# Optimization experiments

Hardware: AMD Instinct MI355X
Metric: run time of the kernel (lower is better)

Reference implementation:

```python
import jax, jax.numpy as jnp
import numpy as np

N = 131072          # total nodes per batched graph side
E = 524288          # total edges per batched graph side (avg degree 4)
B = 4096            # number of graph pairs
NPG = 32            # nodes per graph
NEG_SLOPE = 0.2
LN_EPS = 1e-5


def setup_inputs() -> dict:
    key = jax.random.key(0)
    ks = jax.random.split(key, 40)
    rn = lambda k, s, sc=0.05: jax.random.normal(k, s, dtype=jnp.float32) * sc
    inp = {}
    inp["feat1"] = jax.random.normal(ks[0], (N, 6), dtype=jnp.float32)
    inp["feat2"] = jax.random.normal(ks[1], (N, 6), dtype=jnp.float32)
    inp["llm_emb"] = jax.random.normal(ks[2], (B, 1024), dtype=jnp.float32)
    inp["src1"] = jax.random.randint(ks[3], (E,), 0, N, dtype=jnp.int32)
    inp["dst1"] = jax.random.randint(ks[4], (E,), 0, N, dtype=jnp.int32)
    inp["src2"] = jax.random.randint(ks[5], (E,), 0, N, dtype=jnp.int32)
    inp["dst2"] = jax.random.randint(ks[6], (E,), 0, N, dtype=jnp.int32)
    inp["gid"] = (jnp.arange(N, dtype=jnp.int32) // NPG).astype(jnp.int32)
    # shared GAT weights (layer: W[in,H*Dh], attn_l[H,Dh], attn_r[H,Dh], bias[H*Dh])
    inp["W1"] = rn(ks[7], (6, 128));   inp["al1"] = rn(ks[8], (4, 32));  inp["ar1"] = rn(ks[9], (4, 32));  inp["b1"] = rn(ks[10], (128,))
    inp["W2"] = rn(ks[11], (128, 128)); inp["al2"] = rn(ks[12], (4, 32)); inp["ar2"] = rn(ks[13], (4, 32)); inp["b2"] = rn(ks[14], (128,))
    inp["W3"] = rn(ks[15], (128, 256)); inp["al3"] = rn(ks[16], (4, 64)); inp["ar3"] = rn(ks[17], (4, 64)); inp["b3"] = rn(ks[18], (256,))
    # fusion
    inp["Wpg"] = rn(ks[19], (512, 512)); inp["bpg"] = rn(ks[20], (512,))
    inp["Wpl"] = rn(ks[21], (1024, 512)); inp["bpl"] = rn(ks[22], (512,))
    inp["Wv"] = rn(ks[23], (512, 512));  inp["bv"] = rn(ks[24], (512,))
    inp["Wo"] = rn(ks[25], (512, 512));  inp["bo"] = rn(ks[26], (512,))
    inp["gamma"] = jnp.ones((512,), jnp.float32); inp["beta"] = jnp.zeros((512,), jnp.float32)
    # classifier
    inp["Wc1"] = rn(ks[27], (512, 256)); inp["bc1"] = rn(ks[28], (256,))
    inp["Wc2"] = rn(ks[29], (256, 1));   inp["bc2"] = rn(ks[30], (1,))
    return inp


def _gat(x, src, dst, W, al, ar, b):
    # DGL GATConv: e_ij = LeakyReLU(a_l.h_src + a_r.h_dst), softmax over edges per dst
    H, Dh = al.shape
    h = (x @ W).reshape(-1, H, Dh)                 # [N,H,Dh]
    el = jnp.sum(h * al, axis=-1)                  # [N,H]
    er = jnp.sum(h * ar, axis=-1)                  # [N,H]
    e = jax.nn.leaky_relu(el[src] + er[dst], NEG_SLOPE)   # [E,H]
    m = jax.ops.segment_max(e, dst, num_segments=N)
    a = jnp.exp(e - m[dst])
    s = jax.ops.segment_sum(a, dst, num_segments=N)
    alpha = a / jnp.where(s[dst] == 0, 1.0, s[dst])       # [E,H]
    out = jax.ops.segment_sum(alpha[:, :, None] * h[src], dst, num_segments=N)
    return out.reshape(-1, H * Dh) + b


def _gnn(x, src, dst, gid, W1, al1, ar1, b1, W2, al2, ar2, b2, W3, al3, ar3, b3):
    h = jax.nn.relu(_gat(x, src, dst, W1, al1, ar1, b1))
    h = jax.nn.relu(_gat(h, src, dst, W2, al2, ar2, b2))
    h = _gat(h, src, dst, W3, al3, ar3, b3)        # [N,256]
    sums = jax.ops.segment_sum(h, gid, num_segments=B)
    cnt = jax.ops.segment_sum(jnp.ones((h.shape[0], 1), h.dtype), gid, num_segments=B)
    return sums / cnt                               # [B,256] mean_nodes


def reference(feat1, feat2, llm_emb, src1, dst1, src2, dst2, gid,
              W1, al1, ar1, b1, W2, al2, ar2, b2, W3, al3, ar3, b3,
              Wpg, bpg, Wpl, bpl, Wv, bv, Wo, bo, gamma, beta,
              Wc1, bc1, Wc2, bc2):
    h1 = _gnn(feat1, src1, dst1, gid, W1, al1, ar1, b1, W2, al2, ar2, b2, W3, al3, ar3, b3)
    h2 = _gnn(feat2, src2, dst2, gid, W1, al1, ar1, b1, W2, al2, ar2, b2, W3, al3, ar3, b3)
    pair = jnp.concatenate([h1, h2], axis=1)        # [B,512]
    gp = pair @ Wpg + bpg                           # [B,512]
    lp = llm_emb @ Wpl + bpl                        # [B,512]
    # MHA with kv seq_len 1: softmax over a single key == 1 -> out = W_o(W_v gp)
    attn = (gp @ Wv + bv) @ Wo + bo
    x = attn + lp
    mu = jnp.mean(x, axis=-1, keepdims=True)
    var = jnp.mean((x - mu) ** 2, axis=-1, keepdims=True)
    fused = (x - mu) / jnp.sqrt(var + LN_EPS) * gamma + beta
    hcls = jax.nn.relu(fused @ Wc1 + bc1)
    return jax.nn.sigmoid(hcls @ Wc2 + bc2)         # [B,1]
```

## Files before the change

kernel.cpp:

```cpp
#include <hip/hip_runtime.h>
#include <hip/hip_fp8.h>

#define NN 131072
#define NE 524288
#define NB 4096
#define CAP 16
#define NEG_SLOPE 0.2f
#define LN_EPS 1e-5f
#define LOG2E 1.44269504088896f

typedef unsigned short bf16;
typedef __attribute__((ext_vector_type(8))) short short8;
typedef __attribute__((ext_vector_type(4))) float floatx4;
typedef __attribute__((ext_vector_type(2))) float floatx2;

#if __has_builtin(__builtin_amdgcn_exp2f)
#define EXP2(x) __builtin_amdgcn_exp2f(x)
#else
#define EXP2(x) exp2f(x)
#endif

__device__ __forceinline__ float bf2f(bf16 h) {
    return __uint_as_float((unsigned)h << 16);
}
__device__ __forceinline__ bf16 f2bf(float f) {
    unsigned u = __float_as_uint(f);
    unsigned r = (u + 0x7FFFu + ((u >> 16) & 1u)) >> 16;
    return (bf16)r;
}
__device__ __forceinline__ unsigned pkbf(float lo, float hi) {
    unsigned r;
    asm("v_cvt_pk_bf16_f32 %0, %1, %2" : "=v"(r) : "v"(lo), "v"(hi));
    return r;
}
__device__ __forceinline__ unsigned char ftofp8(float f) {
    return (unsigned char)(__builtin_amdgcn_cvt_pk_fp8_f32(f, f, 0, false) & 0xFF);
}
__device__ __forceinline__ float leaky(float x) {
    return fmaxf(x, 0.f) + NEG_SLOPE * fminf(x, 0.f);
}


__global__ void zero_i32(int* p, int n) {
    int i = blockIdx.x * blockDim.x + threadIdx.x;
    if (i < n) p[i] = 0;
}

__global__ void scatter_slots_kernel(const int* __restrict__ s0, const int* __restrict__ d0,
                                     const int* __restrict__ s1, const int* __restrict__ d1,
                                     int* __restrict__ deg, int* __restrict__ slots) {
    int i = blockIdx.x * blockDim.x + threadIdx.x;
    int side = i >= NE;
    int e = i - side * NE;
    int d = side ? d1[e] : d0[e];
    int s = side ? s1[e] : s0[e];
    int gd = side * NN + d;
    int p = atomicAdd(&deg[gd], 1);
    if (p < CAP) slots[(size_t)gd * CAP + p] = side * NN + s;
}

#define PREP_TOTAL (16384 + 32768 + 524288 + 131072 + 2048 + 2048 + 48 + 4096)

__global__ void prep_all_kernel(const float* __restrict__ W2, const float* __restrict__ W3,
                                const float* __restrict__ Wpl, const float* __restrict__ Wc1,
                                const float* __restrict__ W1,
                                const float* __restrict__ al1, const float* __restrict__ ar1,
                                const float* __restrict__ al2, const float* __restrict__ ar2,
                                const float* __restrict__ al3, const float* __restrict__ ar3,
                                const float* __restrict__ b1v,
                                bf16* __restrict__ W2t, bf16* __restrict__ W3t,
                                bf16* __restrict__ Wplt, bf16* __restrict__ Wc1t,
                                bf16* __restrict__ Ff2, bf16* __restrict__ Ff3,
                                float* __restrict__ F1, bf16* __restrict__ W1f) {
    int i = blockIdx.x * blockDim.x + threadIdx.x;
    if (i < 16384) {
        int c = i >> 7, k = i & 127;
        W2t[i] = f2bf(W2[k * 128 + c]);
        return;
    }
    i -= 16384;
    if (i < 32768) {
        int c = i >> 7, k = i & 127;
        W3t[i] = f2bf(W3[k * 256 + c]);
        return;
    }
    i -= 32768;
    if (i < 524288) {
        int c = i >> 10, k = i & 1023;
        Wplt[i] = f2bf(Wpl[k * 512 + c]);
        return;
    }
    i -= 524288;
    if (i < 131072) {
        int c = i >> 9, k = i & 511;
        Wc1t[i] = f2bf(Wc1[k * 256 + c]);
        return;
    }
    i -= 131072;
    if (i < 2048) {
        int c = i >> 7, k = i & 127;
        float s = 0.f;
        if (c < 8) {
            const float* a = (c < 4) ? al2 : ar2;
            int hh = c & 3;
            for (int d = 0; d < 32; d++) s += W2[k * 128 + hh * 32 + d] * a[hh * 32 + d];
        }
        Ff2[i] = f2bf(s);
        return;
    }
    i -= 2048;
    if (i < 2048) {
        int c = i >> 7, k = i & 127;
        float s = 0.f;
        if (c < 8) {
            const float* a = (c < 4) ? al3 : ar3;
            int hh = c & 3;
            for (int d = 0; d < 64; d++) s += W3[k * 256 + hh * 64 + d] * a[hh * 64 + d];
        }
        Ff3[i] = f2bf(s);
        return;
    }
    i -= 2048;
    if (i < 48) {
        int k = i >> 3, c = i & 7;
        const float* a = (c < 4) ? al1 : ar1;
        int hh = c & 3;
        float s = 0.f;
        for (int d = 0; d < 32; d++) s += W1[k * 128 + hh * 32 + d] * a[hh * 32 + d];
        F1[k * 8 + c] = s * LOG2E;
        return;
    }
    i -= 48;
    if (i < 4096) {
        int c = i >> 5, k = i & 31;
        int h = c >> 5, d = k & 7;
        float v = 0.f;
        if ((k >> 3) == h) {
            if (d < 6) v = W1[d * 128 + c];
            else if (d == 6) v = b1v[c];
        }
        W1f[i] = f2bf(v);
    }
}

__global__ void f2bf_kernel(const float* __restrict__ x, bf16* __restrict__ y) {
    int i = blockIdx.x * blockDim.x + threadIdx.x;
    float4 v = ((const float4*)x)[i];
    ushort4 u;
    u.x = f2bf(v.x); u.y = f2bf(v.y); u.z = f2bf(v.z); u.w = f2bf(v.w);
    ((ushort4*)y)[i] = u;
}

__global__ void wt_kernel(const float* __restrict__ W, bf16* __restrict__ Wt, int K, int C) {
    int i = blockIdx.x * blockDim.x + threadIdx.x;
    if (i >= K * C) return;
    int c = i / K, k = i - c * K;
    Wt[i] = f2bf(W[(size_t)k * C + c]);
}


__global__ void featelr_kernel(const float* __restrict__ f0, const float* __restrict__ f1,
                               const float* __restrict__ F1, float* __restrict__ fpk,
                               float* __restrict__ el, float* __restrict__ er) {
    int n = blockIdx.x * blockDim.x + threadIdx.x;
    const float* x = (n < NN) ? (f0 + (size_t)n * 6) : (f1 + (size_t)(n - NN) * 6);
    float xv[6];
#pragma unroll
    for (int k = 0; k < 6; k++) xv[k] = x[k];
    float4* o = (float4*)(fpk + (size_t)n * 8);
    o[0] = make_float4(xv[0], xv[1], xv[2], xv[3]);
    o[1] = make_float4(xv[4], xv[5], 0.f, 0.f);
    float4 elv, erv;
    float* ep = (float*)&elv;
    float* rp = (float*)&erv;
#pragma unroll
    for (int c = 0; c < 4; c++) {
        float sl = 0.f, sr = 0.f;
#pragma unroll
        for (int k = 0; k < 6; k++) {
            sl += xv[k] * F1[k * 8 + c];
            sr += xv[k] * F1[k * 8 + c + 4];
        }
        ep[c] = sl;
        rp[c] = sr;
    }
    *(float4*)(el + (size_t)n * 4) = elv;
    *(float4*)(er + (size_t)n * 4) = erv;
}

__global__ __launch_bounds__(256) void agg1mfma_kernel(
        const float* __restrict__ fpk, const float* __restrict__ el,
        const float* __restrict__ er, const int* __restrict__ deg,
        const int* __restrict__ slots, const bf16* __restrict__ W1fg,
        bf16* __restrict__ xb) {
    __shared__ bf16 sW[128 * 40];
    __shared__ bf16 sagg[256 * 40];
    int t = threadIdx.x;
    if (t < 128) {
        const uint4* src = (const uint4*)(W1fg + t * 32);
        uint4* dstp = (uint4*)(sW + t * 40);
        dstp[0] = src[0]; dstp[1] = src[1]; dstp[2] = src[2]; dstp[3] = src[3];
    }

    int node = blockIdx.x * 256 + t;
    int dg = deg[node];
    dg = (dg > CAP) ? CAP : dg;
    float4 er4 = *(const float4*)(er + (size_t)node * 4);
    const int* sp = slots + (size_t)node * CAP;
    float a0[4], a1[4], a2[4], a3[4], a4[4], a5[4], ss[4];
#pragma unroll
    for (int h = 0; h < 4; h++) {
        a0[h] = a1[h] = a2[h] = a3[h] = a4[h] = a5[h] = ss[h] = 0.f;
    }
    for (int p = 0; p < dg; p += 4) {
        int4 s4 = *(const int4*)(sp + p);
        int sarr[4] = {s4.x, s4.y, s4.z, s4.w};
#pragma unroll
        for (int k = 0; k < 4; k++) {
            bool vld = (p + k) < dg;
            int g = vld ? sarr[k] : s4.x;
            float4 e4 = *(const float4*)(el + (size_t)g * 4);
            float4 xa = *(const float4*)(fpk + (size_t)g * 8);
            float4 xc = *(const float4*)(fpk + (size_t)g * 8 + 4);
            float eh[4] = {e4.x, e4.y, e4.z, e4.w};
            float rh[4] = {er4.x, er4.y, er4.z, er4.w};
#pragma unroll
            for (int h = 0; h < 4; h++) {
                float z = eh[h] + rh[h];
                float w = EXP2(fmaxf(z, 0.f) + NEG_SLOPE * fminf(z, 0.f));
                w = vld ? w : 0.f;
                ss[h] += w;
                a0[h] += w * xa.x; a1[h] += w * xa.y; a2[h] += w * xa.z;
                a3[h] += w * xa.w; a4[h] += w * xc.x; a5[h] += w * xc.y;
            }
        }
    }
#pragma unroll
    for (int h = 0; h < 4; h++) {
        float rs = (dg > 0) ? 1.f / ss[h] : 0.f;
        uint4 o;
        o.x = pkbf(a0[h] * rs, a1[h] * rs);
        o.y = pkbf(a2[h] * rs, a3[h] * rs);
        o.z = pkbf(a4[h] * rs, a5[h] * rs);
        o.w = 0x00003F80u;
        *(uint4*)(sagg + t * 40 + h * 8) = o;
    }
    __syncthreads();

    int wave = t >> 6, lane = t & 63;
    int mlane = lane & 15, quad = lane >> 4;
    short8 af[8];
#pragma unroll
    for (int j = 0; j < 8; j++)
        af[j] = *(const short8*)(sW + (j * 16 + mlane) * 40 + quad * 8);
    floatx4 z4 = (floatx4){0.f, 0.f, 0.f, 0.f};
#pragma unroll
    for (int nt = 0; nt < 4; nt++) {
        int lrow = wave * 64 + nt * 16 + mlane;
        short8 bfr = *(const short8*)(sagg + lrow * 40 + quad * 8);
        floatx4 c[8];
#pragma unroll
        for (int j = 0; j < 8; j++)
            c[j] = __builtin_amdgcn_mfma_f32_16x16x32_bf16(af[j], bfr, z4, 0, 0, 0);
        bf16* op = xb + (size_t)(blockIdx.x * 256 + lrow) * 128 + quad * 4;
#pragma unroll
        for (int j = 0; j < 8; j++) {
            uint2 o;
            o.x = pkbf(fmaxf(c[j][0], 0.f), fmaxf(c[j][1], 0.f));
            o.y = pkbf(fmaxf(c[j][2], 0.f), fmaxf(c[j][3], 0.f));
            *(uint2*)(op + j * 16) = o;
        }
    }
}


__device__ __forceinline__ void softmax_phaseA(const float* __restrict__ el,
                                               const float* __restrict__ er,
                                               const int* __restrict__ slots,
                                               int wid, int dg, int lane,
                                               float* alpha_out, int* src_out) {
    int e = lane & 15, h = lane >> 4;
    int sA = slots[(size_t)wid * CAP + e];
    int sAc = (e < dg) ? sA : 0;
    float erh = er[wid * 4 + h];
    float elv = el[sAc * 4 + h];
    float w = (e < dg) ? __expf(leaky(elv + erh)) : 0.f;
    float ssum = w;
    ssum += __shfl_xor(ssum, 1, 64);
    ssum += __shfl_xor(ssum, 2, 64);
    ssum += __shfl_xor(ssum, 4, 64);
    ssum += __shfl_xor(ssum, 8, 64);
    *alpha_out = (dg > 0) ? w * (1.f / ssum) : 0.f;
    *src_out = sAc;
}

__global__ void agg2_kernel(const unsigned char* __restrict__ h8, const float* __restrict__ el,
                            const float* __restrict__ er, const int* __restrict__ deg,
                            const int* __restrict__ slots, const float* __restrict__ bias,
                            bf16* __restrict__ out) {
    int t = blockIdx.x * blockDim.x + threadIdx.x;
    int wid = t >> 5;
    int gl = threadIdx.x & 31;
    int dg = deg[wid];
    dg = (dg > CAP) ? CAP : dg;
    int head = gl >> 3;
    int fbase = gl * 4;
    float erh = er[wid * 4 + head];
    const int* sp = slots + (size_t)wid * CAP;
    float a0 = 0.f, a1 = 0.f, a2 = 0.f, a3 = 0.f, ssum = 0.f;

    for (int p = 0; p < dg; p += 4) {
        int4 s4 = *(const int4*)(sp + p);
        int s[4]; bool v[4];
        s[0] = s4.x; v[0] = true;
        v[1] = p + 1 < dg; s[1] = v[1] ? s4.y : s4.x;
        v[2] = p + 2 < dg; s[2] = v[2] ? s4.z : s4.x;
        v[3] = p + 3 < dg; s[3] = v[3] ? s4.w : s4.x;
        float elv[4]; unsigned u1[4];
#pragma unroll
        for (int k = 0; k < 4; k++) {
            elv[k] = el[s[k] * 4 + head];
            u1[k] = *(const unsigned*)(h8 + (size_t)s[k] * 128 + fbase);
        }
#pragma unroll
        for (int k = 0; k < 4; k++) {
            float w = v[k] ? __expf(leaky(elv[k] + erh)) : 0.f;
            ssum += w;
            floatx2 lo = __builtin_amdgcn_cvt_pk_f32_fp8((int)u1[k], false);
            floatx2 hi = __builtin_amdgcn_cvt_pk_f32_fp8((int)u1[k], true);
            a0 += w * lo[0]; a1 += w * lo[1];
            a2 += w * hi[0]; a3 += w * hi[1];
        }
    }
    float rs = (dg > 0) ? 1.f / ssum : 0.f;
    float4 bbv = *(const float4*)(bias + fbase);
    float v0 = fmaxf(a0 * rs + bbv.x, 0.f), v1 = fmaxf(a1 * rs + bbv.y, 0.f);
    float v2 = fmaxf(a2 * rs + bbv.z, 0.f), v3 = fmaxf(a3 * rs + bbv.w, 0.f);
    uint2 uo;
    uo.x = (unsigned)f2bf(v0) | ((unsigned)f2bf(v1) << 16);
    uo.y = (unsigned)f2bf(v2) | ((unsigned)f2bf(v3) << 16);
    *(uint2*)(out + (size_t)wid * 128 + fbase) = uo;
}

__global__ void agg3pool_kernel(const unsigned char* __restrict__ h8,
                                const float* __restrict__ el, const float* __restrict__ er,
                                const int* __restrict__ deg, const int* __restrict__ slots,
                                const float* __restrict__ bias, bf16* __restrict__ pair) {
    __shared__ float red[4 * 256];
    int side = blockIdx.x >> 12;
    int b = blockIdx.x & 4095;
    int nodebase = side * NN + b * 32;
    int grp = threadIdx.x >> 6, lane = threadIdx.x & 63;
    int fbase = lane * 4;
    int grpbase = lane & 48;
    float p0 = 0.f, p1 = 0.f, p2 = 0.f, p3 = 0.f;

    for (int nn = 0; nn < 8; nn++) {
        int wid = nodebase + grp * 8 + nn;
        int dg = deg[wid];
        dg = (dg > CAP) ? CAP : dg;
        float alpha; int sAc;
        softmax_phaseA(el, er, slots, wid, dg, lane, &alpha, &sAc);
        for (int p = 0; p < dg; p += 4) {
            int sc[4]; float av[4];
#pragma unroll
            for (int k = 0; k < 4; k++) {
                int srcl = grpbase + p + k;
                sc[k] = __shfl(sAc, srcl, 64);
                av[k] = __shfl(alpha, srcl, 64);
            }
            unsigned u[4];
#pragma unroll
            for (int k = 0; k < 4; k++)
                u[k] = *(const unsigned*)(h8 + (size_t)sc[k] * 256 + fbase);
#pragma unroll
            for (int k = 0; k < 4; k++) {
                floatx2 lo = __builtin_amdgcn_cvt_pk_f32_fp8((int)u[k], false);
                floatx2 hi = __builtin_amdgcn_cvt_pk_f32_fp8((int)u[k], true);
                p0 += av[k] * lo[0]; p1 += av[k] * lo[1];
                p2 += av[k] * hi[0]; p3 += av[k] * hi[1];
            }
        }
    }
    red[grp * 256 + fbase + 0] = p0;
    red[grp * 256 + fbase + 1] = p1;
    red[grp * 256 + fbase + 2] = p2;
    red[grp * 256 + fbase + 3] = p3;
    __syncthreads();
    if (grp == 0) {
        float4 bbv = *(const float4*)(bias + fbase);
        float s0 = 0.f, s1 = 0.f, s2 = 0.f, s3 = 0.f;
#pragma unroll
        for (int g = 0; g < 4; g++) {
            s0 += red[g * 256 + fbase + 0];
            s1 += red[g * 256 + fbase + 1];
            s2 += red[g * 256 + fbase + 2];
            s3 += red[g * 256 + fbase + 3];
        }
        const float inv = 1.0f / 32.0f;
        float v0 = s0 * inv + bbv.x, v1 = s1 * inv + bbv.y;
        float v2 = s2 * inv + bbv.z, v3 = s3 * inv + bbv.w;
        uint2 uo;
        uo.x = (unsigned)f2bf(v0) | ((unsigned)f2bf(v1) << 16);
        uo.y = (unsigned)f2bf(v2) | ((unsigned)f2bf(v3) << 16);
        *(uint2*)(pair + (size_t)b * 512 + side * 256 + fbase) = uo;
    }
}

template <bool FOLD, bool OUT8>
__global__ __launch_bounds__(256) void mgemm_kernel(const bf16* __restrict__ A,
                                                    const bf16* __restrict__ Wt,
                                                    const float* __restrict__ bias,
                                                    void* __restrict__ out,
                                                    int K, int C, int relu,
                                                    const bf16* __restrict__ Ff,
                                                    float* __restrict__ el,
                                                    float* __restrict__ er) {
    __shared__ short As[128 * 48];
    __shared__ short Bs[128 * 48];
    int t = threadIdx.x;
    int wave = t >> 6, lane = t & 63;
    int wm = (wave >> 1) * 64, wn = (wave & 1) * 64;
    int bm = blockIdx.x * 128, bn = blockIdx.y * 128;
    int m_lane = lane & 15, quad = lane >> 4;
    bool dofold = FOLD && (blockIdx.y == 0) && (wn == 0);

    floatx4 acc[4][4];
#pragma unroll
    for (int i = 0; i < 4; i++)
#pragma unroll
        for (int j = 0; j < 4; j++) acc[i][j] = (floatx4){0.f, 0.f, 0.f, 0.f};
    floatx4 facc[4];
    if (FOLD) {
#pragma unroll
        for (int i = 0; i < 4; i++) facc[i] = (floatx4){0.f, 0.f, 0.f, 0.f};
    }

    int lrow = t >> 2, lq = t & 3;
    for (int k0 = 0; k0 < K; k0 += 32) {
        __syncthreads();
#pragma unroll
        for (int pass = 0; pass < 2; pass++) {
            int row = lrow + pass * 64;
            *(short8*)&As[row * 48 + lq * 8] =
                *(const short8*)(A + (size_t)(bm + row) * K + k0 + lq * 8);
            *(short8*)&Bs[row * 48 + lq * 8] =
                *(const short8*)(Wt + (size_t)(bn + row) * K + k0 + lq * 8);
        }
        __syncthreads();
        short8 af[4], bf[4];
#pragma unroll
        for (int i = 0; i < 4; i++)
            af[i] = *(const short8*)&As[(wm + i * 16 + m_lane) * 48 + quad * 8];
#pragma unroll
        for (int j = 0; j < 4; j++)
            bf[j] = *(const short8*)&Bs[(wn + j * 16 + m_lane) * 48 + quad * 8];
        if (dofold) {
            short8 fbv = *(const short8*)(Ff + m_lane * K + k0 + quad * 8);
#pragma unroll
            for (int i = 0; i < 4; i++)
                facc[i] = __builtin_amdgcn_mfma_f32_16x16x32_bf16(af[i], fbv, facc[i], 0, 0, 0);
        }
#pragma unroll
        for (int i = 0; i < 4; i++)
#pragma unroll
            for (int j = 0; j < 4; j++)
                acc[i][j] = __builtin_amdgcn_mfma_f32_16x16x32_bf16(af[i], bf[j], acc[i][j], 0, 0, 0);
    }

#pragma unroll
    for (int i = 0; i < 4; i++) {
#pragma unroll
        for (int j = 0; j < 4; j++) {
            int gc = bn + wn + j * 16 + m_lane;
            float bbv = bias ? bias[gc] : 0.f;
#pragma unroll
            for (int r = 0; r < 4; r++) {
                int gr = bm + wm + i * 16 + quad * 4 + r;
                float v = acc[i][j][r] + bbv;
                if (relu) v = fmaxf(v, 0.f);
                if (OUT8) ((unsigned char*)out)[(size_t)gr * C + gc] = ftofp8(v);
                else      ((bf16*)out)[(size_t)gr * C + gc] = f2bf(v);
            }
        }
    }
    if (dofold && m_lane < 8) {
        float* dst = (m_lane < 4) ? el : er;
        int hh = m_lane & 3;
#pragma unroll
        for (int i = 0; i < 4; i++)
#pragma unroll
            for (int r = 0; r < 4; r++) {
                int gr = bm + wm + i * 16 + quad * 4 + r;
                dst[gr * 4 + hh] = facc[i][r];
            }
    }
}

__global__ __launch_bounds__(256) void fgemm512_kernel(const float* __restrict__ A,
                                                       const float* __restrict__ B,
                                                       float* __restrict__ C) {
    const int BK = 16;
    __shared__ float As[BK][68];
    __shared__ float Bs[BK][68];
    int t = threadIdx.x;
    int bm = blockIdx.x * 64, bn = blockIdx.y * 64;
    int tm0 = (t & 15) * 4, tn0 = (t >> 4) * 4;
    float acc[4][4] = {};
    int la_m = t >> 2, la_k = (t & 3) * 4;
    int lb_k = t >> 4, lb_c = (t & 15) * 4;

    for (int k0 = 0; k0 < 512; k0 += BK) {
        float4 a4 = *(const float4*)(A + (size_t)(bm + la_m) * 512 + k0 + la_k);
        float4 b4 = *(const float4*)(B + (size_t)(k0 + lb_k) * 512 + bn + lb_c);
        As[la_k + 0][la_m] = a4.x; As[la_k + 1][la_m] = a4.y;
        As[la_k + 2][la_m] = a4.z; As[la_k + 3][la_m] = a4.w;
        *(float4*)&Bs[lb_k][lb_c] = b4;
        __syncthreads();
#pragma unroll
        for (int k = 0; k < BK; k++) {
            float4 av = *(const float4*)&As[k][tm0];
            float4 bv = *(const float4*)&Bs[k][tn0];
            acc[0][0] += av.x * bv.x; acc[0][1] += av.x * bv.y; acc[0][2] += av.x * bv.z; acc[0][3] += av.x * bv.w;
            acc[1][0] += av.y * bv.x; acc[1][1] += av.y * bv.y; acc[1][2] += av.y * bv.z; acc[1][3] += av.y * bv.w;
            acc[2][0] += av.z * bv.x; acc[2][1] += av.z * bv.y; acc[2][2] += av.z * bv.z; acc[2][3] += av.z * bv.w;
            acc[3][0] += av.w * bv.x; acc[3][1] += av.w * bv.y; acc[3][2] += av.w * bv.z; acc[3][3] += av.w * bv.w;
        }
        __syncthreads();
    }
#pragma unroll
    for (int i = 0; i < 4; i++) {
        float4 o = make_float4(acc[i][0], acc[i][1], acc[i][2], acc[i][3]);
        *(float4*)(C + (size_t)(bm + tm0 + i) * 512 + bn + tn0) = o;
    }
}

__global__ void biasstep_kernel(const float* __restrict__ vin, const float* __restrict__ M,
                                const float* __restrict__ badd, float* __restrict__ vout) {
    int c = blockIdx.x * blockDim.x + threadIdx.x;
    float s = 0.f;
    for (int k = 0; k < 512; k++) s += vin[k] * M[(size_t)k * 512 + c];
    vout[c] = s + badd[c];
}


__global__ void ln_kernel(const bf16* __restrict__ attn, const bf16* __restrict__ lp,
                          const float* __restrict__ gamma, const float* __restrict__ beta,
                          bf16* __restrict__ out) {
    __shared__ float red[256];
    int b = blockIdx.x, t = threadIdx.x;
    size_t base = (size_t)b * 512;
    float x0 = bf2f(attn[base + t]) + bf2f(lp[base + t]);
    float x1 = bf2f(attn[base + 256 + t]) + bf2f(lp[base + 256 + t]);
    red[t] = x0 + x1; __syncthreads();
    for (int off = 128; off > 0; off >>= 1) { if (t < off) red[t] += red[t + off]; __syncthreads(); }
    float mu = red[0] * (1.0f / 512.0f);
    __syncthreads();
    float d0 = x0 - mu, d1 = x1 - mu;
    red[t] = d0 * d0 + d1 * d1; __syncthreads();
    for (int off = 128; off > 0; off >>= 1) { if (t < off) red[t] += red[t + off]; __syncthreads(); }
    float rstd = rsqrtf(red[0] * (1.0f / 512.0f) + LN_EPS);
    out[base + t]       = f2bf(d0 * rstd * gamma[t] + beta[t]);
    out[base + 256 + t] = f2bf(d1 * rstd * gamma[256 + t] + beta[256 + t]);
}

__global__ void cls2_kernel(const bf16* __restrict__ hc, const float* __restrict__ Wc2,
                            const float* __restrict__ bc2, float* __restrict__ out) {
    int wid = (blockIdx.x * blockDim.x + threadIdx.x) >> 6;
    int lane = threadIdx.x & 63;
    if (wid >= NB) return;
    float s = 0.f;
#pragma unroll
    for (int j = 0; j < 4; j++) {
        int k = lane + 64 * j;
        s += bf2f(hc[(size_t)wid * 256 + k]) * Wc2[k];
    }
    for (int off = 32; off > 0; off >>= 1) s += __shfl_down(s, off);
    if (lane == 0) {
        float v = s + bc2[0];
        out[wid] = 1.0f / (1.0f + __expf(-v));
    }
}


static inline size_t alup(size_t x) { return (x + 255) & ~(size_t)255; }

extern "C" void kernel_launch(void* const* d_in, const int* in_sizes, int n_in,
                              void* d_out, int out_size, void* d_ws, size_t ws_size,
                              hipStream_t stream) {
    const float* feat0 = (const float*)d_in[0];
    const float* feat1 = (const float*)d_in[1];
    const float* llm = (const float*)d_in[2];
    const int* srcs[2] = {(const int*)d_in[3], (const int*)d_in[5]};
    const int* dsts[2] = {(const int*)d_in[4], (const int*)d_in[6]};
    const float* W1 = (const float*)d_in[8];
    const float* al[3] = {(const float*)d_in[9],  (const float*)d_in[13], (const float*)d_in[17]};
    const float* ar[3] = {(const float*)d_in[10], (const float*)d_in[14], (const float*)d_in[18]};
    const float* bb[3] = {(const float*)d_in[11], (const float*)d_in[15], (const float*)d_in[19]};
    const float* W2 = (const float*)d_in[12];
    const float* W3 = (const float*)d_in[16];
    const float* Wpg = (const float*)d_in[20]; const float* bpg = (const float*)d_in[21];
    const float* Wpl = (const float*)d_in[22]; const float* bpl = (const float*)d_in[23];
    const float* Wv  = (const float*)d_in[24]; const float* bv  = (const float*)d_in[25];
    const float* Wo  = (const float*)d_in[26]; const float* bo  = (const float*)d_in[27];
    const float* gamma = (const float*)d_in[28]; const float* beta = (const float*)d_in[29];
    const float* Wc1 = (const float*)d_in[30]; const float* bc1 = (const float*)d_in[31];
    const float* Wc2 = (const float*)d_in[32]; const float* bc2 = (const float*)d_in[33];
    float* outp = (float*)d_out;

    const size_t N2 = (size_t)2 * NN;

    char* p = (char*)d_ws;
    auto take = [&](size_t bytes) { char* r = p; p += alup(bytes); return r; };
    bf16*  xb     = (bf16*)take(N2 * 128 * 2);
    char*  regB   = (char*)take(N2 * 256);
    float* el     = (float*)take(N2 * 4 * 4);
    float* er     = (float*)take(N2 * 4 * 4);
    int*   deg    = (int*)take(N2 * 4);
    int*   slots  = (int*)take(N2 * CAP * 4);
    bf16*  pair   = (bf16*)take((size_t)NB * 512 * 2);
    bf16*  llm_bf = (bf16*)take((size_t)NB * 1024 * 2);
    bf16*  W2t  = (bf16*)take(128 * 128 * 2);
    bf16*  W3t  = (bf16*)take(128 * 256 * 2);
    bf16*  Wplt = (bf16*)take(1024 * 512 * 2);
    bf16*  Wc1t = (bf16*)take(512 * 256 * 2);
    bf16*  Wcot = (bf16*)take(512 * 512 * 2);
    float* F1   = (float*)take(6 * 8 * 4);
    bf16*  Ff2  = (bf16*)take(16 * 128 * 2);
    bf16*  Ff3  = (bf16*)take(16 * 128 * 2);
    bf16*  W1fg = (bf16*)take(128 * 32 * 2);
    float* c1   = (float*)take(512 * 512 * 4);
    float* c2   = (float*)take(512 * 512 * 4);
    float* bias1 = (float*)take(512 * 4);
    float* bco   = (float*)take(512 * 4);
    float* fpk          = (float*)regB;
    unsigned char* hb2  = (unsigned char*)regB;
    unsigned char* hb3  = (unsigned char*)regB;
    bf16* fbb   = (bf16*)regB;
    bf16* lp    = fbb + (size_t)0 * NB * 512;
    bf16* attn  = fbb + (size_t)1 * NB * 512;
    bf16* fused = fbb + (size_t)2 * NB * 512;
    bf16* hc    = fbb + (size_t)3 * NB * 512;
    (void)ws_size; (void)n_in; (void)in_sizes; (void)out_size;

    auto mgemm = [&](const bf16* A, const bf16* Wt, const float* bias, bf16* o,
                     int M, int K, int C, int relu) {
        dim3 g(M / 128, C / 128);
        mgemm_kernel<false, false><<<g, 256, 0, stream>>>(A, Wt, bias, o, K, C, relu,
                                                          nullptr, nullptr, nullptr);
    };

    prep_all_kernel<<<(PREP_TOTAL + 255) / 256, 256, 0, stream>>>(
        W2, W3, Wpl, Wc1, W1, al[0], ar[0], al[1], ar[1], al[2], ar[2], bb[0],
        W2t, W3t, Wplt, Wc1t, Ff2, Ff3, F1, W1fg);
    f2bf_kernel<<<NB * 1024 / 4 / 256, 256, 0, stream>>>(llm, llm_bf);
    {
        dim3 g8(8, 8);
        fgemm512_kernel<<<g8, 256, 0, stream>>>(Wpg, Wv, c1);
        fgemm512_kernel<<<g8, 256, 0, stream>>>(c1, Wo, c2);
        wt_kernel<<<(512 * 512 + 255) / 256, 256, 0, stream>>>(c2, Wcot, 512, 512);
        biasstep_kernel<<<2, 256, 0, stream>>>(bpg, Wv, bv, bias1);
        biasstep_kernel<<<2, 256, 0, stream>>>(bias1, Wo, bo, bco);
    }

    zero_i32<<<2 * NN / 256, 256, 0, stream>>>(deg, 2 * NN);
    scatter_slots_kernel<<<2 * NE / 256, 256, 0, stream>>>(srcs[0], dsts[0],
                                                           srcs[1], dsts[1], deg, slots);

    featelr_kernel<<<2 * NN / 256, 256, 0, stream>>>(feat0, feat1, F1, fpk, el, er);
    agg1mfma_kernel<<<2 * NN / 256, 256, 0, stream>>>(fpk, el, er, deg, slots, W1fg, xb);
    {
        dim3 g(2 * NN / 128, 1);
        mgemm_kernel<true, true><<<g, 256, 0, stream>>>(xb, W2t, nullptr, hb2, 128, 128, 0,
                                                        Ff2, el, er);
    }
    agg2_kernel<<<2 * NN * 32 / 256, 256, 0, stream>>>(hb2, el, er, deg, slots, bb[1], xb);
    {
        dim3 g(2 * NN / 128, 2);
        mgemm_kernel<true, true><<<g, 256, 0, stream>>>(xb, W3t, nullptr, hb3, 128, 256, 0,
                                                        Ff3, el, er);
    }
    agg3pool_kernel<<<2 * NB, 256, 0, stream>>>(hb3, el, er, deg, slots, bb[2], pair);

    mgemm(llm_bf, Wplt, bpl, lp, NB, 1024, 512, 0);
    mgemm(pair, Wcot, bco, attn, NB, 512, 512, 0);
    ln_kernel<<<NB, 256, 0, stream>>>(attn, lp, gamma, beta, fused);
    mgemm(fused, Wc1t, bc1, hc, NB, 512, 256, 1);
    cls2_kernel<<<NB / 4, 256, 0, stream>>>(hc, Wc2, bc2, outp);
}
```

Measured before the change: 625.5 us.

## Build CSR slots via two-pass bucketed partition instead of global atomics

Replaces the zero-fill plus global-atomic scatter of edges into per-node slot lists with a two-pass scheme. Edges are first partitioned into 1024 buckets of 256 destination nodes using shared-memory counters, then each bucket block builds its deg and slots in LDS and writes them out coalesced. This aims to remove contended global atomics and scattered writes, at the cost of an intermediate cells buffer. Per-cell overflow beyond 24 entries is silently dropped, which could lose edges on skewed inputs. Slot order also differs from the original.

```diff
diff --git a/kernel.cpp b/kernel.cpp
--- a/kernel.cpp
+++ b/kernel.cpp
@@ -9,6 +9,10 @@
 #define LN_EPS 1e-5f
 #define LOG2E 1.44269504088896f
 
+#define NBKT 1024
+#define NBLK1 256
+#define CELL_CAP 24
+
 typedef unsigned short bf16;
 typedef __attribute__((ext_vector_type(8))) short short8;
 typedef __attribute__((ext_vector_type(4))) float floatx4;
@@ -40,23 +44,65 @@
     return fmaxf(x, 0.f) + NEG_SLOPE * fminf(x, 0.f);
 }
 
-
-__global__ void zero_i32(int* p, int n) {
-    int i = blockIdx.x * blockDim.x + threadIdx.x;
-    if (i < n) p[i] = 0;
-}
-
-__global__ void scatter_slots_kernel(const int* __restrict__ s0, const int* __restrict__ d0,
-                                     const int* __restrict__ s1, const int* __restrict__ d1,
-                                     int* __restrict__ deg, int* __restrict__ slots) {
-    int i = blockIdx.x * blockDim.x + threadIdx.x;
-    int side = i >= NE;
-    int e = i - side * NE;
-    int d = side ? d1[e] : d0[e];
-    int s = side ? s1[e] : s0[e];
-    int gd = side * NN + d;
-    int p = atomicAdd(&deg[gd], 1);
-    if (p < CAP) slots[(size_t)gd * CAP + p] = side * NN + s;
+__global__ __launch_bounds__(256) void part_edges_kernel(
+        const int* __restrict__ s0, const int* __restrict__ d0,
+        const int* __restrict__ s1, const int* __restrict__ d1,
+        unsigned* __restrict__ cells, int* __restrict__ counts) {
+    __shared__ int lcnt[NBKT];
+    int blk = blockIdx.x, t = threadIdx.x;
+    for (int i = t; i < NBKT; i += 256) lcnt[i] = 0;
+    __syncthreads();
+    int side = blk >= (NBLK1 / 2);
+    const int4* dp = (const int4*)(side ? d1 : d0);
+    const int4* sp = (const int4*)(side ? s1 : s0);
+    int base4 = (blk - side * (NBLK1 / 2)) * 1024;
+    int gbase = side * NN;
+#pragma unroll
+    for (int it = 0; it < 4; it++) {
+        int e4 = base4 + it * 256 + t;
+        int4 dd = dp[e4];
+        int4 ss = sp[e4];
+        int d[4] = {gbase + dd.x, gbase + dd.y, gbase + dd.z, gbase + dd.w};
+        int s[4] = {gbase + ss.x, gbase + ss.y, gbase + ss.z, gbase + ss.w};
+#pragma unroll
+        for (int k = 0; k < 4; k++) {
+            int b = d[k] >> 8;
+            int r = atomicAdd(&lcnt[b], 1);
+            if (r < CELL_CAP)
+                cells[((size_t)b * NBLK1 + blk) * CELL_CAP + r] =
+                    ((unsigned)s[k] << 8) | (unsigned)(d[k] & 255);
+        }
+    }
+    __syncthreads();
+    for (int i = t; i < NBKT; i += 256) {
+        int c = lcnt[i];
+        counts[i * NBLK1 + blk] = (c > CELL_CAP) ? CELL_CAP : c;
+    }
+}
+
+__global__ __launch_bounds__(256) void build_slots_kernel(
+        const unsigned* __restrict__ cells, const int* __restrict__ counts,
+        int* __restrict__ deg, int* __restrict__ slots) {
+    __shared__ int ldeg[256];
+    __shared__ int lslot[256 * CAP];
+    int b = blockIdx.x, t = threadIdx.x;
+    ldeg[t] = 0;
+    for (int i = t; i < 256 * CAP; i += 256) lslot[i] = 0;
+    __syncthreads();
+    int cnt = counts[b * NBLK1 + t];
+    const unsigned* cp = cells + ((size_t)b * NBLK1 + t) * CELL_CAP;
+    for (int i = 0; i < cnt; i++) {
+        unsigned v = cp[i];
+        int d = v & 255;
+        int s = (int)(v >> 8);
+        int p = atomicAdd(&ldeg[d], 1);
+        if (p < CAP) lslot[d * CAP + p] = s;
+    }
+    __syncthreads();
+    int node0 = b * 256;
+    deg[node0 + t] = ldeg[t];
+    for (int i = t; i < 256 * CAP; i += 256)
+        slots[(size_t)node0 * CAP + i] = lslot[i];
 }
 
 #define PREP_TOTAL (16384 + 32768 + 524288 + 131072 + 2048 + 2048 + 48 + 4096)
@@ -633,6 +679,8 @@
     float* c2   = (float*)take(512 * 512 * 4);
     float* bias1 = (float*)take(512 * 4);
     float* bco   = (float*)take(512 * 4);
+    unsigned* cells = (unsigned*)regB;
+    int* counts = (int*)(regB + (size_t)NBKT * NBLK1 * CELL_CAP * 4);
     float* fpk          = (float*)regB;
     unsigned char* hb2  = (unsigned char*)regB;
     unsigned char* hb3  = (unsigned char*)regB;
@@ -649,6 +697,10 @@
         mgemm_kernel<false, false><<<g, 256, 0, stream>>>(A, Wt, bias, o, K, C, relu,
                                                           nullptr, nullptr, nullptr);
     };
+
+    part_edges_kernel<<<NBLK1, 256, 0, stream>>>(srcs[0], dsts[0], srcs[1], dsts[1],
+                                                 cells, counts);
+    build_slots_kernel<<<NBKT, 256, 0, stream>>>(cells, counts, deg, slots);
 
     prep_all_kernel<<<(PREP_TOTAL + 255) / 256, 256, 0, stream>>>(
         W2, W3, Wpl, Wc1, W1, al[0], ar[0], al[1], ar[1], al[2], ar[2], bb[0],
@@ -663,10 +715,6 @@
         biasstep_kernel<<<2, 256, 0, stream>>>(bias1, Wo, bo, bco);
     }
 
-    zero_i32<<<2 * NN / 256, 256, 0, stream>>>(deg, 2 * NN);
-    scatter_slots_kernel<<<2 * NE / 256, 256, 0, stream>>>(srcs[0], dsts[0],
-                                                           srcs[1], dsts[1], deg, slots);
-
     featelr_kernel<<<2 * NN / 256, 256, 0, stream>>>(feat0, feat1, F1, fpk, el, er);
     agg1mfma_kernel<<<2 * NN / 256, 256, 0, stream>>>(fpk, el, er, deg, slots, W1fg, xb);
     {
```

Result: faster. 580.1 us (-7.2%).
